# Kernel optimization log

Measured on AMD Instinct MI355X. Metric: run time of the kernel, lower is better.

The kernel has to match this reference:

```python
import jax, jax.numpy as jnp
import numpy as np

MARGIN = 0.2
BETA = 0.8333333
EPS = 1e-8          # torch cosine_similarity eps
BIG = 1.0e9         # sentinel used by the torch code for masking

B, M, FEAT, RES = 64, 2048, 512, 32


def setup_inputs() -> dict:
    key = jax.random.key(0)
    k1, k2, k3, k4 = jax.random.split(key, 4)
    return {
        "anchor_features": jax.random.normal(k1, (B, FEAT), dtype=jnp.float32),
        "true_voxels": jax.random.uniform(k2, (B, RES, RES, RES), dtype=jnp.float32),
        "memory_keys": jax.random.normal(k3, (M, FEAT), dtype=jnp.float32),
        "memory_values": jax.random.uniform(k4, (M, RES, RES, RES), dtype=jnp.float32),
    }


def reference(anchor_features, true_voxels, memory_keys, memory_values):
    b = true_voxels.shape[0]
    m = memory_values.shape[0]
    v = true_voxels.reshape(b, -1)        # (B, N) with N = res^3
    w = memory_values.reshape(m, -1)      # (M, N)
    n = v.shape[1]

    # Pairwise voxel MSE via ||a||^2 - 2ab + ||b||^2 GEMM trick (same math,
    # avoids the (B, M, N) broadcast intermediate).
    v_sq = jnp.sum(v * v, axis=1)                         # (B,)
    w_sq = jnp.sum(w * w, axis=1)                         # (M,)
    mse = (v_sq[:, None] + w_sq[None, :] - 2.0 * (v @ w.T)) / n   # (B, M)
    sv_scores = 1.0 - mse

    pos_mask = sv_scores > BETA
    neg_mask = sv_scores < BETA

    # Pairwise cosine distance 1 - cos_sim (norms clamped at eps like torch).
    a_norm = jnp.maximum(jnp.linalg.norm(anchor_features, axis=1, keepdims=True), EPS)
    k_norm = jnp.maximum(jnp.linalg.norm(memory_keys, axis=1, keepdims=True), EPS)
    key_dists = 1.0 - (anchor_features / a_norm) @ (memory_keys / k_norm).T  # (B, M)

    hardest_pos = jnp.max(jnp.where(pos_mask, key_dists, -BIG), axis=1)  # (B,)
    hardest_neg = jnp.min(jnp.where(neg_mask, key_dists, BIG), axis=1)   # (B,)

    loss = jnp.maximum(hardest_pos - hardest_neg + MARGIN, 0.0)          # (B,)

    valid = jnp.any(pos_mask, axis=1) & jnp.any(neg_mask, axis=1)        # (B,)
    cnt = jnp.sum(valid.astype(loss.dtype))
    total = jnp.sum(jnp.where(valid, loss, 0.0))
    # Masked mean; 0.0 when no valid triplets (mirrors the torch early-return).
    return jnp.where(cnt > 0, total / jnp.maximum(cnt, 1.0), 0.0)
```

## Files before the change

### kernel.cpp

```cpp
#include <hip/hip_runtime.h>


typedef __attribute__((ext_vector_type(8)))  short bf16x8;
typedef __attribute__((ext_vector_type(16))) float f32x16;

constexpr int   Mdim   = 2048;
constexpr int   Nvox   = 32768;
constexpr int   NS     = 16;
constexpr float BETA   = 0.8333333f;
constexpr float MARGIN = 0.2f;
constexpr float BIGV   = 1.0e9f;

constexpr size_t OFF_VSQP = 0;
constexpr size_t OFF_AINV = 1024;
constexpr size_t OFF_KINV = 1088;
constexpr size_t OFF_WSQ  = 3136;
constexpr size_t OFF_WSQP = 5184;
constexpr size_t OFF_PHP  = 37952;
constexpr size_t OFF_PHN  = 38208;
constexpr size_t OFF_PAP  = 38464;
constexpr size_t OFF_PAN  = 38720;
constexpr size_t OFF_KEYP = 38976;
constexpr size_t OFF_DOTP = 170048;
constexpr size_t OFF_VHI  = 2267200;
constexpr size_t OFF_VLO  = 3315776;

__device__ __forceinline__ unsigned int bf16rne(float x) {
    unsigned int u = __float_as_uint(x);
    return (u + 0x7FFFu + ((u >> 16) & 1u)) >> 16;
}
__device__ __forceinline__ int pk2(unsigned int lo, unsigned int hi) {
    return (int)(lo | (hi << 16));
}
__device__ __forceinline__ void async16(const ushort* g, ushort* l) {
    __builtin_amdgcn_global_load_lds(
        (const __attribute__((address_space(1))) unsigned int*)g,
        (__attribute__((address_space(3))) unsigned int*)l, 16, 0, 0);
}

__global__ __launch_bounds__(256) void prep_kernel(
    const float* __restrict__ vox, const float* __restrict__ anc,
    const float* __restrict__ keys,
    ushort* __restrict__ vhi, ushort* __restrict__ vlo,
    float* __restrict__ vsqp, float* __restrict__ ainv, float* __restrict__ kinv)
{
    const int tid = threadIdx.x;
    if (blockIdx.x < 256) {
        const int bg = blockIdx.x >> 4;
        const int ks = blockIdx.x & 15;
        const int bsub = tid & 3;
        const int b  = bg * 4 + bsub;
        const int kw = tid >> 2;
        float sq = 0.f;
        #pragma unroll
        for (int it = 0; it < 2; ++it) {
            const int kloc = ks * 2048 + (it * 64 + kw) * 16;
            const float4* src = reinterpret_cast<const float4*>(vox + (size_t)b * Nvox + kloc);
            float4 x[4];
            #pragma unroll
            for (int j = 0; j < 4; ++j) x[j] = src[j];
            unsigned int h[16], l[16];
            #pragma unroll
            for (int j = 0; j < 4; ++j) {
                const float e[4] = {x[j].x, x[j].y, x[j].z, x[j].w};
                #pragma unroll
                for (int q = 0; q < 4; ++q) {
                    const float v = e[q];
                    sq = fmaf(v, v, sq);
                    const unsigned int hb = bf16rne(v);
                    h[j*4+q] = hb;
                    const float r = v - __uint_as_float(hb << 16);
                    l[j*4+q] = bf16rne(r);
                }
            }
            const int c = kloc >> 6, s = (kloc >> 4) & 3;
            const size_t base = (size_t)c * 4096 + (b >> 5) * 2048 + s * 512 + (b & 31) * 8;
            int4 hp0 = { pk2(h[0],h[1]), pk2(h[2],h[3]), pk2(h[4],h[5]), pk2(h[6],h[7]) };
            int4 hp1 = { pk2(h[8],h[9]), pk2(h[10],h[11]), pk2(h[12],h[13]), pk2(h[14],h[15]) };
            int4 lp0 = { pk2(l[0],l[1]), pk2(l[2],l[3]), pk2(l[4],l[5]), pk2(l[6],l[7]) };
            int4 lp1 = { pk2(l[8],l[9]), pk2(l[10],l[11]), pk2(l[12],l[13]), pk2(l[14],l[15]) };
            *reinterpret_cast<int4*>(vhi + base)       = hp0;
            *reinterpret_cast<int4*>(vhi + base + 256) = hp1;
            *reinterpret_cast<int4*>(vlo + base)       = lp0;
            *reinterpret_cast<int4*>(vlo + base + 256) = lp1;
        }
        #pragma unroll
        for (int off = 32; off >= 4; off >>= 1) sq += __shfl_down(sq, off);
        __shared__ float red[16];
        const int lane = tid & 63, wave = tid >> 6;
        if (lane < 4) red[wave * 4 + lane] = sq;
        __syncthreads();
        if (tid < 4)
            vsqp[(size_t)(bg * 4 + tid) * 16 + ks] =
                red[tid] + red[tid + 4] + red[tid + 8] + red[tid + 12];
    } else {
        const int r = (blockIdx.x - 256) * 4 + (tid >> 6);
        const int lane = tid & 63;
        const float* src = (r < 64) ? (anc + (size_t)r * 512)
                                    : (keys + (size_t)(r - 64) * 512);
        const float4* s4 = reinterpret_cast<const float4*>(src);
        float4 x = s4[lane];
        float4 y = s4[lane + 64];
        float p = 0.f;
        p = fmaf(x.x, x.x, p); p = fmaf(x.y, x.y, p);
        p = fmaf(x.z, x.z, p); p = fmaf(x.w, x.w, p);
        p = fmaf(y.x, y.x, p); p = fmaf(y.y, y.y, p);
        p = fmaf(y.z, y.z, p); p = fmaf(y.w, y.w, p);
        #pragma unroll
        for (int off = 32; off > 0; off >>= 1) p += __shfl_down(p, off);
        if (lane == 0) {
            float inv = 1.f / fmaxf(sqrtf(p), 1e-8f);
            if (r < 64) ainv[r] = inv; else kinv[r - 64] = inv;
        }
    }
}

__global__ __launch_bounds__(256) void gemm_big(
    const ushort* __restrict__ vhi, const ushort* __restrict__ vlo,
    const float* __restrict__ W,
    float* __restrict__ dotp, float* __restrict__ wsqp)
{
    __shared__ ushort sVhi[4096], sVlo[4096], sWhi[4096];
    __shared__ float red[256];

    const int tid  = threadIdx.x;
    const int lane = tid & 63;
    const int wave = tid >> 6;
    const int mb   = blockIdx.x & 31;
    const int ns   = blockIdx.x >> 5;
    const int srow = tid >> 2;
    const int sq   = tid & 3;

    const float*  wptr = W + (size_t)(mb * 64 + srow) * Nvox + ns * 2048 + sq * 16;
    const ushort* vhig = vhi + (size_t)(ns * 32) * 4096 + wave * 1024 + lane * 8;
    const ushort* vlog = vlo + (size_t)(ns * 32) * 4096 + wave * 1024 + lane * 8;
    ushort* ldsVhi = &sVhi[wave * 1024];
    ushort* ldsVlo = &sVlo[wave * 1024];

    const int wr = wave >> 1, wc = wave & 1;
    f32x16 acc = {};
    float wsq = 0.f;

    float4 wreg[4];
    #pragma unroll
    for (int j = 0; j < 4; ++j) wreg[j] = *reinterpret_cast<const float4*>(wptr + j * 4);

    const int woff0 = (srow >> 5) * 2048 + sq * 512 + (srow & 31) * 8;

    for (int ch = 0; ch < 32; ++ch) {
        int4 p0, p1;
        {
            unsigned int hb[16];
            #pragma unroll
            for (int j = 0; j < 4; ++j) {
                const float e[4] = {wreg[j].x, wreg[j].y, wreg[j].z, wreg[j].w};
                #pragma unroll
                for (int q = 0; q < 4; ++q) {
                    wsq = fmaf(e[q], e[q], wsq);
                    hb[j*4+q] = bf16rne(e[q]);
                }
            }
            p0 = (int4){ pk2(hb[0],hb[1]), pk2(hb[2],hb[3]), pk2(hb[4],hb[5]), pk2(hb[6],hb[7]) };
            p1 = (int4){ pk2(hb[8],hb[9]), pk2(hb[10],hb[11]), pk2(hb[12],hb[13]), pk2(hb[14],hb[15]) };
        }
        __syncthreads();
        async16(vhig + (size_t)ch * 4096,       ldsVhi);
        async16(vhig + (size_t)ch * 4096 + 512, ldsVhi + 512);
        async16(vlog + (size_t)ch * 4096,       ldsVlo);
        async16(vlog + (size_t)ch * 4096 + 512, ldsVlo + 512);
        *reinterpret_cast<int4*>(&sWhi[woff0])       = p0;
        *reinterpret_cast<int4*>(&sWhi[woff0 + 256]) = p1;
        if (ch < 31) {
            #pragma unroll
            for (int j = 0; j < 4; ++j)
                wreg[j] = *reinterpret_cast<const float4*>(wptr + (ch + 1) * 64 + j * 4);
        }
        __syncthreads();
        #pragma unroll
        for (int s = 0; s < 4; ++s) {
            bf16x8 ah = *reinterpret_cast<const bf16x8*>(&sVhi[wr * 2048 + s * 512 + lane * 8]);
            bf16x8 al = *reinterpret_cast<const bf16x8*>(&sVlo[wr * 2048 + s * 512 + lane * 8]);
            bf16x8 bh = *reinterpret_cast<const bf16x8*>(&sWhi[wc * 2048 + s * 512 + lane * 8]);
            acc = __builtin_amdgcn_mfma_f32_32x32x16_bf16(ah, bh, acc, 0, 0, 0);
            acc = __builtin_amdgcn_mfma_f32_32x32x16_bf16(al, bh, acc, 0, 0, 0);
        }
    }

    const int col   = lane & 31;
    const int rbase = 4 * (lane >> 5);
    const size_t out_m = (size_t)(mb * 64 + wc * 32 + col);
    #pragma unroll
    for (int r = 0; r < 16; ++r) {
        const int row = (r & 3) + 8 * (r >> 2) + rbase;
        const int b   = wr * 32 + row;
        dotp[(size_t)(ns * 64 + b) * Mdim + out_m] = acc[r];
    }
    red[tid] = wsq;
    __syncthreads();
    if (tid < 64)
        wsqp[(size_t)ns * Mdim + mb * 64 + tid] =
            red[tid*4] + red[tid*4+1] + red[tid*4+2] + red[tid*4+3];
}

__global__ __launch_bounds__(256) void keydist_kernel(
    const float* __restrict__ anc, const float* __restrict__ keys,
    const float* __restrict__ wsqp, float* __restrict__ keyp,
    float* __restrict__ wsq)
{
    const int tid = threadIdx.x;
    if (blockIdx.x >= 256) {
        const int m = (blockIdx.x - 256) * 256 + tid;
        float s = 0.f;
        #pragma unroll
        for (int sp = 0; sp < NS; ++sp) s += wsqp[(size_t)sp * Mdim + m];
        wsq[m] = s;
        return;
    }
    __shared__ float kk[8 * 516];
    const int mt = blockIdx.x * 8;
    {
        const int row = tid >> 5, colb = (tid & 31) * 16;
        const float4* src = reinterpret_cast<const float4*>(keys + (size_t)(mt + row) * 512 + colb);
        #pragma unroll
        for (int j = 0; j < 4; ++j)
            *reinterpret_cast<float4*>(&kk[row * 516 + colb + j * 4]) = src[j];
    }
    __syncthreads();
    const int b = tid >> 2, msub = tid & 3;
    const float* arow = anc + (size_t)b * 512;
    const float* k0 = &kk[msub * 516];
    const float* k1 = &kk[(msub + 4) * 516];
    float d0 = 0.f, d1 = 0.f;
    for (int k = 0; k < 512; k += 4) {
        const float4 a = *reinterpret_cast<const float4*>(arow + k);
        const float4 x = *reinterpret_cast<const float4*>(k0 + k);
        const float4 y = *reinterpret_cast<const float4*>(k1 + k);
        d0 = fmaf(a.x, x.x, d0); d0 = fmaf(a.y, x.y, d0);
        d0 = fmaf(a.z, x.z, d0); d0 = fmaf(a.w, x.w, d0);
        d1 = fmaf(a.x, y.x, d1); d1 = fmaf(a.y, y.y, d1);
        d1 = fmaf(a.z, y.z, d1); d1 = fmaf(a.w, y.w, d1);
    }
    keyp[(size_t)b * Mdim + mt + msub]     = d0;
    keyp[(size_t)b * Mdim + mt + msub + 4] = d1;
}

__global__ __launch_bounds__(256) void rowpart_kernel(
    const float* __restrict__ dotp, const float* __restrict__ wsq,
    const float* __restrict__ keyp, const float* __restrict__ vsqp,
    const float* __restrict__ ainv, const float* __restrict__ kinv,
    float* __restrict__ php, float* __restrict__ phn,
    float* __restrict__ pap, float* __restrict__ pan)
{
    const int bid = blockIdx.x, tid = threadIdx.x;
    const int b = bid >> 2, sl = bid & 3;
    float vs = 0.f;
    #pragma unroll
    for (int i = 0; i < 16; ++i) vs += vsqp[(size_t)b * 16 + i];
    const float ai = ainv[b];
    float hp = -BIGV, hn = BIGV, ap = 0.f, an = 0.f;
    #pragma unroll
    for (int rep = 0; rep < 2; ++rep) {
        const int m = sl * 512 + rep * 256 + tid;
        float dot = 0.f;
        #pragma unroll
        for (int s = 0; s < NS; ++s) dot += dotp[(size_t)(s * 64 + b) * Mdim + m];
        const float sv = 1.f - (vs + wsq[m] - 2.f * dot) * (1.f / 32768.f);
        const float kd = 1.f - keyp[(size_t)b * Mdim + m] * ai * kinv[m];
        if (sv > BETA) { ap = 1.f; hp = fmaxf(hp, kd); }
        if (sv < BETA) { an = 1.f; hn = fminf(hn, kd); }
    }
    #pragma unroll
    for (int off = 32; off > 0; off >>= 1) {
        hp = fmaxf(hp, __shfl_down(hp, off));
        hn = fminf(hn, __shfl_down(hn, off));
        ap = fmaxf(ap, __shfl_down(ap, off));
        an = fmaxf(an, __shfl_down(an, off));
    }
    __shared__ float sb[16];
    const int wv = tid >> 6;
    if ((tid & 63) == 0) {
        sb[wv * 4 + 0] = hp; sb[wv * 4 + 1] = hn;
        sb[wv * 4 + 2] = ap; sb[wv * 4 + 3] = an;
    }
    __syncthreads();
    if (tid == 0) {
        for (int w2 = 1; w2 < 4; ++w2) {
            hp = fmaxf(hp, sb[w2 * 4 + 0]);
            hn = fminf(hn, sb[w2 * 4 + 1]);
            ap = fmaxf(ap, sb[w2 * 4 + 2]);
            an = fmaxf(an, sb[w2 * 4 + 3]);
        }
        php[bid] = hp; phn[bid] = hn; pap[bid] = ap; pan[bid] = an;
    }
}

__global__ void final_kernel(const float* __restrict__ php, const float* __restrict__ phn,
                             const float* __restrict__ pap, const float* __restrict__ pan,
                             float* __restrict__ out)
{
    const int t = threadIdx.x;
    float hp = php[t], hn = phn[t], ap = pap[t], an = pan[t];
    hp = fmaxf(hp, __shfl_down(hp, 2)); hp = fmaxf(hp, __shfl_down(hp, 1));
    hn = fminf(hn, __shfl_down(hn, 2)); hn = fminf(hn, __shfl_down(hn, 1));
    ap = fmaxf(ap, __shfl_down(ap, 2)); ap = fmaxf(ap, __shfl_down(ap, 1));
    an = fmaxf(an, __shfl_down(an, 2)); an = fmaxf(an, __shfl_down(an, 1));
    __shared__ float sl[64], sc[64];
    if ((t & 3) == 0) {
        const int b = t >> 2;
        const float valid = (ap > 0.f && an > 0.f) ? 1.f : 0.f;
        sl[b] = fmaxf(hp - hn + MARGIN, 0.f) * valid;
        sc[b] = valid;
    }
    __syncthreads();
    if (t < 64) {
        float l = sl[t], c = sc[t];
        #pragma unroll
        for (int off = 32; off > 0; off >>= 1) {
            l += __shfl_down(l, off);
            c += __shfl_down(c, off);
        }
        if (t == 0) out[0] = (c > 0.f) ? (l / c) : 0.f;
    }
}

extern "C" void kernel_launch(void* const* d_in, const int* in_sizes, int n_in,
                              void* d_out, int out_size, void* d_ws, size_t ws_size,
                              hipStream_t stream) {
    const float* anchor = (const float*)d_in[0];
    const float* voxels = (const float*)d_in[1];
    const float* keys   = (const float*)d_in[2];
    const float* vals   = (const float*)d_in[3];

    float* ws = (float*)d_ws;
    float*  vsqp = ws + OFF_VSQP;
    float*  ainv = ws + OFF_AINV;
    float*  kinv = ws + OFF_KINV;
    float*  wsq  = ws + OFF_WSQ;
    float*  wsqp = ws + OFF_WSQP;
    float*  php  = ws + OFF_PHP;
    float*  phn  = ws + OFF_PHN;
    float*  pap  = ws + OFF_PAP;
    float*  pan  = ws + OFF_PAN;
    float*  keyp = ws + OFF_KEYP;
    float*  dotp = ws + OFF_DOTP;
    ushort* vhi  = (ushort*)(ws + OFF_VHI);
    ushort* vlo  = (ushort*)(ws + OFF_VLO);

    prep_kernel<<<784, 256, 0, stream>>>(voxels, anchor, keys, vhi, vlo, vsqp, ainv, kinv);
    gemm_big<<<32 * NS, 256, 0, stream>>>(vhi, vlo, vals, dotp, wsqp);
    keydist_kernel<<<264, 256, 0, stream>>>(anchor, keys, wsqp, keyp, wsq);
    rowpart_kernel<<<256, 256, 0, stream>>>(dotp, wsq, keyp, vsqp, ainv, kinv,
                                            php, phn, pap, pan);
    final_kernel<<<1, 256, 0, stream>>>(php, phn, pap, pan, (float*)d_out);
}
```

Baseline: 411.5 us.

## Fuse keydist into prep, wsq reduction into rowpart, final into last block

Moves the anchor-key dot product blocks into the prep kernel as extra blocks, folds the wsq partial-sum reduction into rowpart, and replaces the final kernel with a last-block-done pattern using an atomic counter reset in prep. This cuts the launch sequence from five kernels to three, removing launch and inter-kernel gaps. In exchange, rowpart reads the wsq partials redundantly for every b, and correctness now depends on atomics and threadfences.

```diff
diff --git a/kernel.cpp b/kernel.cpp
--- a/kernel.cpp
+++ b/kernel.cpp
@@ -14,16 +14,16 @@
 constexpr size_t OFF_VSQP = 0;
 constexpr size_t OFF_AINV = 1024;
 constexpr size_t OFF_KINV = 1088;
-constexpr size_t OFF_WSQ  = 3136;
-constexpr size_t OFF_WSQP = 5184;
-constexpr size_t OFF_PHP  = 37952;
-constexpr size_t OFF_PHN  = 38208;
-constexpr size_t OFF_PAP  = 38464;
-constexpr size_t OFF_PAN  = 38720;
-constexpr size_t OFF_KEYP = 38976;
-constexpr size_t OFF_DOTP = 170048;
-constexpr size_t OFF_VHI  = 2267200;
-constexpr size_t OFF_VLO  = 3315776;
+constexpr size_t OFF_WSQP = 3136;
+constexpr size_t OFF_PHP  = 35904;
+constexpr size_t OFF_PHN  = 36160;
+constexpr size_t OFF_PAP  = 36416;
+constexpr size_t OFF_PAN  = 36672;
+constexpr size_t OFF_CNT  = 36928;
+constexpr size_t OFF_KEYP = 36992;
+constexpr size_t OFF_DOTP = 168064;
+constexpr size_t OFF_VHI  = 2265216;
+constexpr size_t OFF_VLO  = 3313792;
 
 __device__ __forceinline__ unsigned int bf16rne(float x) {
     unsigned int u = __float_as_uint(x);
@@ -42,10 +42,13 @@
     const float* __restrict__ vox, const float* __restrict__ anc,
     const float* __restrict__ keys,
     ushort* __restrict__ vhi, ushort* __restrict__ vlo,
-    float* __restrict__ vsqp, float* __restrict__ ainv, float* __restrict__ kinv)
+    float* __restrict__ vsqp, float* __restrict__ ainv, float* __restrict__ kinv,
+    float* __restrict__ keyp, int* __restrict__ cnt)
 {
+    __shared__ float kk[8 * 516];
     const int tid = threadIdx.x;
     if (blockIdx.x < 256) {
+        if (blockIdx.x == 0 && tid == 0) cnt[0] = 0;
         const int bg = blockIdx.x >> 4;
         const int ks = blockIdx.x & 15;
         const int bsub = tid & 3;
@@ -86,14 +89,13 @@
         }
         #pragma unroll
         for (int off = 32; off >= 4; off >>= 1) sq += __shfl_down(sq, off);
-        __shared__ float red[16];
         const int lane = tid & 63, wave = tid >> 6;
-        if (lane < 4) red[wave * 4 + lane] = sq;
+        if (lane < 4) kk[wave * 4 + lane] = sq;
         __syncthreads();
         if (tid < 4)
             vsqp[(size_t)(bg * 4 + tid) * 16 + ks] =
-                red[tid] + red[tid + 4] + red[tid + 8] + red[tid + 12];
-    } else {
+                kk[tid] + kk[tid + 4] + kk[tid + 8] + kk[tid + 12];
+    } else if (blockIdx.x < 784) {
         const int r = (blockIdx.x - 256) * 4 + (tid >> 6);
         const int lane = tid & 63;
         const float* src = (r < 64) ? (anc + (size_t)r * 512)
@@ -112,6 +114,33 @@
             float inv = 1.f / fmaxf(sqrtf(p), 1e-8f);
             if (r < 64) ainv[r] = inv; else kinv[r - 64] = inv;
         }
+    } else {
+        const int mt = (blockIdx.x - 784) * 8;
+        {
+            const int row = tid >> 5, colb = (tid & 31) * 16;
+            const float4* src = reinterpret_cast<const float4*>(keys + (size_t)(mt + row) * 512 + colb);
+            #pragma unroll
+            for (int j = 0; j < 4; ++j)
+                *reinterpret_cast<float4*>(&kk[row * 516 + colb + j * 4]) = src[j];
+        }
+        __syncthreads();
+        const int b = tid >> 2, msub = tid & 3;
+        const float* arow = anc + (size_t)b * 512;
+        const float* k0 = &kk[msub * 516];
+        const float* k1 = &kk[(msub + 4) * 516];
+        float d0 = 0.f, d1 = 0.f;
+        #pragma unroll 4
+        for (int k = 0; k < 512; k += 4) {
+            const float4 a = *reinterpret_cast<const float4*>(arow + k);
+            const float4 x = *reinterpret_cast<const float4*>(k0 + k);
+            const float4 y = *reinterpret_cast<const float4*>(k1 + k);
+            d0 = fmaf(a.x, x.x, d0); d0 = fmaf(a.y, x.y, d0);
+            d0 = fmaf(a.z, x.z, d0); d0 = fmaf(a.w, x.w, d0);
+            d1 = fmaf(a.x, y.x, d1); d1 = fmaf(a.y, y.y, d1);
+            d1 = fmaf(a.z, y.z, d1); d1 = fmaf(a.w, y.w, d1);
+        }
+        keyp[(size_t)b * Mdim + mt + msub]     = d0;
+        keyp[(size_t)b * Mdim + mt + msub + 4] = d1;
     }
 }
 
@@ -202,57 +231,16 @@
             red[tid*4] + red[tid*4+1] + red[tid*4+2] + red[tid*4+3];
 }
 
-__global__ __launch_bounds__(256) void keydist_kernel(
-    const float* __restrict__ anc, const float* __restrict__ keys,
-    const float* __restrict__ wsqp, float* __restrict__ keyp,
-    float* __restrict__ wsq)
-{
-    const int tid = threadIdx.x;
-    if (blockIdx.x >= 256) {
-        const int m = (blockIdx.x - 256) * 256 + tid;
-        float s = 0.f;
-        #pragma unroll
-        for (int sp = 0; sp < NS; ++sp) s += wsqp[(size_t)sp * Mdim + m];
-        wsq[m] = s;
-        return;
-    }
-    __shared__ float kk[8 * 516];
-    const int mt = blockIdx.x * 8;
-    {
-        const int row = tid >> 5, colb = (tid & 31) * 16;
-        const float4* src = reinterpret_cast<const float4*>(keys + (size_t)(mt + row) * 512 + colb);
-        #pragma unroll
-        for (int j = 0; j < 4; ++j)
-            *reinterpret_cast<float4*>(&kk[row * 516 + colb + j * 4]) = src[j];
-    }
-    __syncthreads();
-    const int b = tid >> 2, msub = tid & 3;
-    const float* arow = anc + (size_t)b * 512;
-    const float* k0 = &kk[msub * 516];
-    const float* k1 = &kk[(msub + 4) * 516];
-    float d0 = 0.f, d1 = 0.f;
-    for (int k = 0; k < 512; k += 4) {
-        const float4 a = *reinterpret_cast<const float4*>(arow + k);
-        const float4 x = *reinterpret_cast<const float4*>(k0 + k);
-        const float4 y = *reinterpret_cast<const float4*>(k1 + k);
-        d0 = fmaf(a.x, x.x, d0); d0 = fmaf(a.y, x.y, d0);
-        d0 = fmaf(a.z, x.z, d0); d0 = fmaf(a.w, x.w, d0);
-        d1 = fmaf(a.x, y.x, d1); d1 = fmaf(a.y, y.y, d1);
-        d1 = fmaf(a.z, y.z, d1); d1 = fmaf(a.w, y.w, d1);
-    }
-    keyp[(size_t)b * Mdim + mt + msub]     = d0;
-    keyp[(size_t)b * Mdim + mt + msub + 4] = d1;
-}
-
 __global__ __launch_bounds__(256) void rowpart_kernel(
-    const float* __restrict__ dotp, const float* __restrict__ wsq,
+    const float* __restrict__ dotp, const float* __restrict__ wsqp,
     const float* __restrict__ keyp, const float* __restrict__ vsqp,
     const float* __restrict__ ainv, const float* __restrict__ kinv,
     float* __restrict__ php, float* __restrict__ phn,
-    float* __restrict__ pap, float* __restrict__ pan)
+    float* __restrict__ pap, float* __restrict__ pan,
+    int* __restrict__ cnt, float* __restrict__ out)
 {
     const int bid = blockIdx.x, tid = threadIdx.x;
-    const int b = bid >> 2, sl = bid & 3;
+    const int b = bid >> 2, slc = bid & 3;
     float vs = 0.f;
     #pragma unroll
     for (int i = 0; i < 16; ++i) vs += vsqp[(size_t)b * 16 + i];
@@ -260,11 +248,14 @@
     float hp = -BIGV, hn = BIGV, ap = 0.f, an = 0.f;
     #pragma unroll
     for (int rep = 0; rep < 2; ++rep) {
-        const int m = sl * 512 + rep * 256 + tid;
-        float dot = 0.f;
-        #pragma unroll
-        for (int s = 0; s < NS; ++s) dot += dotp[(size_t)(s * 64 + b) * Mdim + m];
-        const float sv = 1.f - (vs + wsq[m] - 2.f * dot) * (1.f / 32768.f);
+        const int m = slc * 512 + rep * 256 + tid;
+        float dot = 0.f, wq = 0.f;
+        #pragma unroll
+        for (int s = 0; s < NS; ++s) {
+            dot += dotp[(size_t)(s * 64 + b) * Mdim + m];
+            wq  += wsqp[(size_t)s * Mdim + m];
+        }
+        const float sv = 1.f - (vs + wq - 2.f * dot) * (1.f / 32768.f);
         const float kd = 1.f - keyp[(size_t)b * Mdim + m] * ai * kinv[m];
         if (sv > BETA) { ap = 1.f; hp = fmaxf(hp, kd); }
         if (sv < BETA) { an = 1.f; hn = fminf(hn, kd); }
@@ -277,6 +268,7 @@
         an = fmaxf(an, __shfl_down(an, off));
     }
     __shared__ float sb[16];
+    __shared__ int isLast;
     const int wv = tid >> 6;
     if ((tid & 63) == 0) {
         sb[wv * 4 + 0] = hp; sb[wv * 4 + 1] = hn;
@@ -290,30 +282,32 @@
             ap = fmaxf(ap, sb[w2 * 4 + 2]);
             an = fmaxf(an, sb[w2 * 4 + 3]);
         }
-        php[bid] = hp; phn[bid] = hn; pap[bid] = ap; pan[bid] = an;
-    }
-}
-
-__global__ void final_kernel(const float* __restrict__ php, const float* __restrict__ phn,
-                             const float* __restrict__ pap, const float* __restrict__ pan,
-                             float* __restrict__ out)
-{
-    const int t = threadIdx.x;
-    float hp = php[t], hn = phn[t], ap = pap[t], an = pan[t];
-    hp = fmaxf(hp, __shfl_down(hp, 2)); hp = fmaxf(hp, __shfl_down(hp, 1));
-    hn = fminf(hn, __shfl_down(hn, 2)); hn = fminf(hn, __shfl_down(hn, 1));
-    ap = fmaxf(ap, __shfl_down(ap, 2)); ap = fmaxf(ap, __shfl_down(ap, 1));
-    an = fmaxf(an, __shfl_down(an, 2)); an = fmaxf(an, __shfl_down(an, 1));
-    __shared__ float sl[64], sc[64];
+        atomicExch(&php[bid], hp); atomicExch(&phn[bid], hn);
+        atomicExch(&pap[bid], ap); atomicExch(&pan[bid], an);
+        __threadfence();
+        const int t = atomicAdd(cnt, 1);
+        isLast = (t == 255);
+    }
+    __syncthreads();
+    if (!isLast) return;
+
+    __threadfence();
+    const int t = tid;
+    float fhp = php[t], fhn = phn[t], fap = pap[t], fan = pan[t];
+    fhp = fmaxf(fhp, __shfl_down(fhp, 2)); fhp = fmaxf(fhp, __shfl_down(fhp, 1));
+    fhn = fminf(fhn, __shfl_down(fhn, 2)); fhn = fminf(fhn, __shfl_down(fhn, 1));
+    fap = fmaxf(fap, __shfl_down(fap, 2)); fap = fmaxf(fap, __shfl_down(fap, 1));
+    fan = fmaxf(fan, __shfl_down(fan, 2)); fan = fmaxf(fan, __shfl_down(fan, 1));
+    __shared__ float fl[64], fc[64];
     if ((t & 3) == 0) {
-        const int b = t >> 2;
-        const float valid = (ap > 0.f && an > 0.f) ? 1.f : 0.f;
-        sl[b] = fmaxf(hp - hn + MARGIN, 0.f) * valid;
-        sc[b] = valid;
+        const int bb = t >> 2;
+        const float valid = (fap > 0.f && fan > 0.f) ? 1.f : 0.f;
+        fl[bb] = fmaxf(fhp - fhn + MARGIN, 0.f) * valid;
+        fc[bb] = valid;
     }
     __syncthreads();
     if (t < 64) {
-        float l = sl[t], c = sc[t];
+        float l = fl[t], c = fc[t];
         #pragma unroll
         for (int off = 32; off > 0; off >>= 1) {
             l += __shfl_down(l, off);
@@ -335,21 +329,20 @@
     float*  vsqp = ws + OFF_VSQP;
     float*  ainv = ws + OFF_AINV;
     float*  kinv = ws + OFF_KINV;
-    float*  wsq  = ws + OFF_WSQ;
     float*  wsqp = ws + OFF_WSQP;
     float*  php  = ws + OFF_PHP;
     float*  phn  = ws + OFF_PHN;
     float*  pap  = ws + OFF_PAP;
     float*  pan  = ws + OFF_PAN;
+    int*    cnt  = (int*)(ws + OFF_CNT);
     float*  keyp = ws + OFF_KEYP;
     float*  dotp = ws + OFF_DOTP;
     ushort* vhi  = (ushort*)(ws + OFF_VHI);
     ushort* vlo  = (ushort*)(ws + OFF_VLO);
 
-    prep_kernel<<<784, 256, 0, stream>>>(voxels, anchor, keys, vhi, vlo, vsqp, ainv, kinv);
+    prep_kernel<<<1040, 256, 0, stream>>>(voxels, anchor, keys, vhi, vlo,
+                                          vsqp, ainv, kinv, keyp, cnt);
     gemm_big<<<32 * NS, 256, 0, stream>>>(vhi, vlo, vals, dotp, wsqp);
-    keydist_kernel<<<264, 256, 0, stream>>>(anchor, keys, wsqp, keyp, wsq);
-    rowpart_kernel<<<256, 256, 0, stream>>>(dotp, wsq, keyp, vsqp, ainv, kinv,
-                                            php, phn, pap, pan);
-    final_kernel<<<1, 256, 0, stream>>>(php, phn, pap, pan, (float*)d_out);
-}
+    rowpart_kernel<<<256, 256, 0, stream>>>(dotp, wsqp, keyp, vsqp, ainv, kinv,
+                                            php, phn, pap, pan, cnt, (float*)d_out);
+}
```

After: 408.5 us (median of 2 runs). No clear change (-0.7%).
